# Performance work log

Measured on AMD Instinct MI355X. Metric: run time of the kernel, lower is better.

The kernel has to match this reference:

```python
import jax, jax.numpy as jnp
import numpy as np

LEVEL = 256
GROUPS = 1
SHIFT = (LEVEL - 1) / 2.0  # symmetric affine shift folded from quant.shift buffer


def qdq(x, clip_val, level=LEVEL, groups=GROUPS, shift=SHIFT):
    """Per-group clip + level quantize-dequantize (what custom_quant.Quant saves/restores).
    clip_val: [groups]. Group split is over equal contiguous chunks of the flattened tensor."""
    shp = x.shape
    xg = x.reshape(groups, -1)
    scale = (2.0 * clip_val) / (level - 1)          # [groups]
    scale = scale.reshape(groups, 1)
    q = jnp.clip(jnp.round(xg / scale + shift), 0.0, level - 1.0)
    return ((q - shift) * scale).reshape(shp)


def setup_inputs() -> dict:
    key = jax.random.key(0)
    k1, k2 = jax.random.split(key)
    # attention-style batched matmul: [B,H,S,Dh] @ [B,H,Dh,S]
    x1 = jax.random.normal(k1, (2, 12, 1024, 64), dtype=jnp.float32)
    x2 = jax.random.normal(k2, (2, 12, 64, 1024), dtype=jnp.float32)
    clip_val1 = 2.0 * jnp.ones((GROUPS,), dtype=jnp.float32)
    clip_val2 = 2.0 * jnp.ones((GROUPS,), dtype=jnp.float32)
    return {"x1": x1, "x2": x2, "clip_val1": clip_val1, "clip_val2": clip_val2}


def reference(x1, x2, clip_val1, clip_val2):
    # Faithful to matmul.forward: the quantized copies are only SAVED for backward;
    # the forward output itself is computed on the full-precision operands.
    # (qdq is exercised in the fwdbwd reference.)
    return jnp.matmul(x1, x2)  # [2,12,1024,1024]
```

## Files before the change

### kernel.cpp

```cpp
#include <hip/hip_runtime.h>
#include <hip/hip_bf16.h>


#define NN 1024

typedef __attribute__((ext_vector_type(4))) float  float4v;
typedef __attribute__((ext_vector_type(8))) short  bf16x8;
typedef __attribute__((ext_vector_type(16))) float floatx16;

__device__ __forceinline__ short f2bs(float f) {
    union { float f; unsigned u; } in;
    in.f = f;
    unsigned u = in.u;
    return (short)((u + 0x7FFFu + ((u >> 16) & 1u)) >> 16);
}


__global__ __launch_bounds__(256) void reformat_AB(const float* __restrict__ A,
                                                   const float* __restrict__ B,
                                                   short* __restrict__ Aw,
                                                   short* __restrict__ Bw) {
    const int bid = blockIdx.x;
    if (bid < 768) {
        int task = bid * 256 + threadIdx.x;
        int bh   = task >> 13;
        int rem  = task & 8191;
        int m    = rem >> 3;
        int kg   = rem & 7;
        const float4v* p = (const float4v*)(A + (size_t)task * 8);
        float4v v0 = __builtin_nontemporal_load(p);
        float4v v1 = __builtin_nontemporal_load(p + 1);
        int ks = kg >> 1, q = kg & 1;
        int mt = m >> 5;
        int lane = (m & 31) + (q << 5);
        size_t dst = ((size_t)((bh * 32 + mt) * 4 + ks)) * 512 + (size_t)lane * 8;
        bf16x8 o;
        o[0] = f2bs(v0.x); o[1] = f2bs(v0.y); o[2] = f2bs(v0.z); o[3] = f2bs(v0.w);
        o[4] = f2bs(v1.x); o[5] = f2bs(v1.y); o[6] = f2bs(v1.z); o[7] = f2bs(v1.w);
        *(bf16x8*)(Aw + dst) = o;
    } else {
        int task = (bid - 768) * 256 + threadIdx.x;
        int kg   = task / 24576;
        int rem  = task - kg * 24576;
        int bh   = rem >> 10;
        int n    = rem & 1023;
        const float* p = B + (size_t)bh * 65536 + (size_t)kg * 8192 + n;
        float v0 = __builtin_nontemporal_load(p + 0 * 1024);
        float v1 = __builtin_nontemporal_load(p + 1 * 1024);
        float v2 = __builtin_nontemporal_load(p + 2 * 1024);
        float v3 = __builtin_nontemporal_load(p + 3 * 1024);
        float v4 = __builtin_nontemporal_load(p + 4 * 1024);
        float v5 = __builtin_nontemporal_load(p + 5 * 1024);
        float v6 = __builtin_nontemporal_load(p + 6 * 1024);
        float v7 = __builtin_nontemporal_load(p + 7 * 1024);
        int ks = kg >> 1, q = kg & 1;
        int nt = n >> 5;
        int lane = (n & 31) + (q << 5);
        size_t dst = ((size_t)((bh * 32 + nt) * 4 + ks)) * 512 + (size_t)lane * 8;
        bf16x8 o;
        o[0] = f2bs(v0); o[1] = f2bs(v1); o[2] = f2bs(v2); o[3] = f2bs(v3);
        o[4] = f2bs(v4); o[5] = f2bs(v5); o[6] = f2bs(v6); o[7] = f2bs(v7);
        *(bf16x8*)(Bw + dst) = o;
    }
}

__global__ __launch_bounds__(256) void bmm_frag(const short* __restrict__ Aw,
                                                const short* __restrict__ Bw,
                                                float* __restrict__ C) {
    const int tid  = threadIdx.x;
    const int lane = tid & 63;
    const int w    = tid >> 6;
    const int bx = blockIdx.x;
    const int by = blockIdx.y;
    const int bh = blockIdx.z;
    const int wm = (w >> 1) * 2;
    const int wn = (w & 1) * 2;

    const short* Ab = Aw + ((size_t)((bh * 32 + by * 4 + wm) * 4)) * 512 + (size_t)lane * 8;
    const short* Bb = Bw + ((size_t)((bh * 32 + bx * 4 + wn) * 4)) * 512 + (size_t)lane * 8;

    floatx16 acc[2][2];
    #pragma unroll
    for (int mi = 0; mi < 2; ++mi)
        #pragma unroll
        for (int ni = 0; ni < 2; ++ni)
            #pragma unroll
            for (int r = 0; r < 16; ++r)
                acc[mi][ni][r] = 0.0f;

    #pragma unroll
    for (int ks = 0; ks < 4; ++ks) {
        bf16x8 a0 = *(const bf16x8*)(Ab + ks * 512);
        bf16x8 a1 = *(const bf16x8*)(Ab + 2048 + ks * 512);
        bf16x8 b0 = *(const bf16x8*)(Bb + ks * 512);
        bf16x8 b1 = *(const bf16x8*)(Bb + 2048 + ks * 512);
        acc[0][0] = __builtin_amdgcn_mfma_f32_32x32x16_bf16(a0, b0, acc[0][0], 0, 0, 0);
        acc[0][1] = __builtin_amdgcn_mfma_f32_32x32x16_bf16(a0, b1, acc[0][1], 0, 0, 0);
        acc[1][0] = __builtin_amdgcn_mfma_f32_32x32x16_bf16(a1, b0, acc[1][0], 0, 0, 0);
        acc[1][1] = __builtin_amdgcn_mfma_f32_32x32x16_bf16(a1, b1, acc[1][1], 0, 0, 0);
    }

    const int nc    = lane & 31;
    const int rbase = (lane >> 5) * 4;
    float* Cb = C + ((size_t)bh << 20)
                  + (size_t)(by * 128 + wm * 32) * NN
                  + bx * 128 + wn * 32 + nc;

    #pragma unroll
    for (int mi = 0; mi < 2; ++mi) {
        #pragma unroll
        for (int ni = 0; ni < 2; ++ni) {
            float* Ct = Cb + (size_t)(mi * 32) * NN + ni * 32;
            #pragma unroll
            for (int r = 0; r < 16; ++r) {
                int row = rbase + (r & 3) + ((r >> 2) * 8);
                Ct[(size_t)row * NN] = acc[mi][ni][r];
            }
        }
    }
}

extern "C" void kernel_launch(void* const* d_in, const int* in_sizes, int n_in,
                              void* d_out, int out_size, void* d_ws, size_t ws_size,
                              hipStream_t stream) {
    const float* x1 = (const float*)d_in[0];
    const float* x2 = (const float*)d_in[1];
    float* out = (float*)d_out;

    short* Aw = (short*)d_ws;
    short* Bw = Aw + 1572864;

    hipLaunchKernelGGL(reformat_AB, dim3(1536), dim3(256), 0, stream, x1, x2, Aw, Bw);
    hipLaunchKernelGGL(bmm_frag, dim3(8, 8, 24), dim3(256), 0, stream, Aw, Bw, out);
}
```

Measured before the change: 121.7 us.

## Compute full 32-row output strips per block with XCD-aware block remap

Replaces the 128x128 tile grid with 768 blocks that each compute a 32x1024 row strip. The A fragment is loaded once per block and reused across 8 N tiles per wave, and a block index swizzle groups blocks for each XCD. Output stores are reordered row-major so each row's eight 32-wide chunks are written together. This trades A-fragment reuse and fewer, larger blocks for higher register pressure (8 accumulators) under a 2-blocks-per-SIMD launch bound.

Result: no change. 121.9 us (+0.2%).

```diff
diff --git a/kernel.cpp b/kernel.cpp
--- a/kernel.cpp
+++ b/kernel.cpp
@@ -64,58 +64,54 @@
     }
 }
 
-__global__ __launch_bounds__(256) void bmm_frag(const short* __restrict__ Aw,
-                                                const short* __restrict__ Bw,
-                                                float* __restrict__ C) {
+__global__ __launch_bounds__(256, 2) void bmm_rows(const short* __restrict__ Aw,
+                                                   const short* __restrict__ Bw,
+                                                   float* __restrict__ C) {
+    const int nid  = blockIdx.x;
+    const int orig = (nid & 7) * 96 + (nid >> 3);
+    const int bh   = orig >> 5;
+    const int ms   = orig & 31;
     const int tid  = threadIdx.x;
     const int lane = tid & 63;
     const int w    = tid >> 6;
-    const int bx = blockIdx.x;
-    const int by = blockIdx.y;
-    const int bh = blockIdx.z;
-    const int wm = (w >> 1) * 2;
-    const int wn = (w & 1) * 2;
 
-    const short* Ab = Aw + ((size_t)((bh * 32 + by * 4 + wm) * 4)) * 512 + (size_t)lane * 8;
-    const short* Bb = Bw + ((size_t)((bh * 32 + bx * 4 + wn) * 4)) * 512 + (size_t)lane * 8;
+    const short* Ab = Aw + ((size_t)((bh * 32 + ms) * 4)) * 512 + (size_t)lane * 8;
+    const short* Bb = Bw + ((size_t)((bh * 32 + w * 8) * 4)) * 512 + (size_t)lane * 8;
 
-    floatx16 acc[2][2];
+    floatx16 acc[8];
     #pragma unroll
-    for (int mi = 0; mi < 2; ++mi)
+    for (int ni = 0; ni < 8; ++ni)
         #pragma unroll
-        for (int ni = 0; ni < 2; ++ni)
-            #pragma unroll
-            for (int r = 0; r < 16; ++r)
-                acc[mi][ni][r] = 0.0f;
+        for (int r = 0; r < 16; ++r)
+            acc[ni][r] = 0.0f;
+
+    bf16x8 a[4];
+    #pragma unroll
+    for (int ks = 0; ks < 4; ++ks)
+        a[ks] = *(const bf16x8*)(Ab + ks * 512);
 
     #pragma unroll
     for (int ks = 0; ks < 4; ++ks) {
-        bf16x8 a0 = *(const bf16x8*)(Ab + ks * 512);
-        bf16x8 a1 = *(const bf16x8*)(Ab + 2048 + ks * 512);
-        bf16x8 b0 = *(const bf16x8*)(Bb + ks * 512);
-        bf16x8 b1 = *(const bf16x8*)(Bb + 2048 + ks * 512);
-        acc[0][0] = __builtin_amdgcn_mfma_f32_32x32x16_bf16(a0, b0, acc[0][0], 0, 0, 0);
-        acc[0][1] = __builtin_amdgcn_mfma_f32_32x32x16_bf16(a0, b1, acc[0][1], 0, 0, 0);
-        acc[1][0] = __builtin_amdgcn_mfma_f32_32x32x16_bf16(a1, b0, acc[1][0], 0, 0, 0);
-        acc[1][1] = __builtin_amdgcn_mfma_f32_32x32x16_bf16(a1, b1, acc[1][1], 0, 0, 0);
+        #pragma unroll
+        for (int ni = 0; ni < 8; ++ni) {
+            bf16x8 b = *(const bf16x8*)(Bb + ni * 2048 + ks * 512);
+            acc[ni] = __builtin_amdgcn_mfma_f32_32x32x16_bf16(a[ks], b, acc[ni], 0, 0, 0);
+        }
     }
 
     const int nc    = lane & 31;
     const int rbase = (lane >> 5) * 4;
     float* Cb = C + ((size_t)bh << 20)
-                  + (size_t)(by * 128 + wm * 32) * NN
-                  + bx * 128 + wn * 32 + nc;
+                  + (size_t)(ms * 32) * NN
+                  + w * 256 + nc;
 
     #pragma unroll
-    for (int mi = 0; mi < 2; ++mi) {
+    for (int rr = 0; rr < 16; ++rr) {
+        int row = rbase + (rr & 3) + ((rr >> 2) * 8);
+        float* Crow = Cb + (size_t)row * NN;
         #pragma unroll
-        for (int ni = 0; ni < 2; ++ni) {
-            float* Ct = Cb + (size_t)(mi * 32) * NN + ni * 32;
-            #pragma unroll
-            for (int r = 0; r < 16; ++r) {
-                int row = rbase + (r & 3) + ((r >> 2) * 8);
-                Ct[(size_t)row * NN] = acc[mi][ni][r];
-            }
+        for (int ni = 0; ni < 8; ++ni) {
+            Crow[ni * 32] = acc[ni][rr];
         }
     }
 }
@@ -131,5 +127,5 @@
     short* Bw = Aw + 1572864;
 
     hipLaunchKernelGGL(reformat_AB, dim3(1536), dim3(256), 0, stream, x1, x2, Aw, Bw);
-    hipLaunchKernelGGL(bmm_frag, dim3(8, 8, 24), dim3(256), 0, stream, Aw, Bw, out);
+    hipLaunchKernelGGL(bmm_rows, dim3(768), dim3(256), 0, stream, Aw, Bw, out);
 }
```
